# Performance work log

Measured on AMD Instinct MI355X. Metric: run time of the kernel, lower is better.

Reference implementation:

```python
import jax, jax.numpy as jnp
import numpy as np

B, S, E = 4, 2048, 512
Q, FFN = 8, 2048


def setup_inputs() -> dict:
    key = jax.random.key(0)
    k_x, k_th, k_w1, k_w2 = jax.random.split(key, 4)
    x = jax.random.normal(k_x, (B, S, E), dtype=jnp.float32)
    # trainable RY angles, one per wire
    theta = jax.random.normal(k_th, (Q,), dtype=jnp.float32)
    W1 = jax.random.normal(k_w1, (Q, FFN), dtype=jnp.float32) / np.sqrt(Q)
    b1 = jnp.zeros((FFN,), dtype=jnp.float32)
    W2 = jax.random.normal(k_w2, (FFN, E), dtype=jnp.float32) / np.sqrt(FFN)
    b2 = jnp.zeros((E,), dtype=jnp.float32)
    return {"x": x, "theta": theta, "W1": W1, "b1": b1, "W2": W2, "b2": b2}


def reference(x, theta, W1, b1, W2, b2):
    # Quantum circuit: |0> -> RX(x_i) -> RY(theta_i) -> <Z> per wire.
    # No entangling gates, so the 8-qubit state factorizes; simulate each
    # qubit's 2 complex amplitudes, batched over all tokens & wires at once.
    n_wires = theta.shape[0]
    xq = x[..., :n_wires]                     # encoder uses input_idx 0..7: [B,S,Q]
    # RX(x)|0> = cos(x/2)|0> - i sin(x/2)|1>
    a = jnp.cos(xq * 0.5).astype(jnp.complex64)
    b = (-1j) * jnp.sin(xq * 0.5).astype(jnp.complex64)
    # RY(theta) = [[c,-s],[s,c]], c=cos(theta/2), s=sin(theta/2)
    c = jnp.cos(theta * 0.5).astype(jnp.complex64)
    s = jnp.sin(theta * 0.5).astype(jnp.complex64)
    a2 = c * a - s * b
    b2_ = s * a + c * b
    # <Z> = |amp0|^2 - |amp1|^2  -> [B,S,Q]
    z = (jnp.abs(a2) ** 2 - jnp.abs(b2_) ** 2).astype(x.dtype)
    # dropout is identity at inference
    h = jax.nn.relu(jnp.einsum('bsq,qf->bsf', z, W1) + b1)
    return jnp.einsum('bsf,fe->bse', h, W2) + b2
```

## Files before the change

kernel.cpp:

```cpp
#include <hip/hip_runtime.h>
#include <hip/hip_bf16.h>

typedef __bf16 bf16_t;
typedef __bf16 bf16x4 __attribute__((ext_vector_type(4)));
typedef __bf16 bf16x8 __attribute__((ext_vector_type(8)));
typedef float f32x4 __attribute__((ext_vector_type(4)));

#define M_TOT 8192
#define N_TOT 512
#define K_TOT 2048
#define E_TOT 512
#define NSEG  16

__device__ __forceinline__ bf16x8 zero8() {
    bf16x8 v;
#pragma unroll
    for (int i = 0; i < 8; ++i) v[i] = (bf16_t)0.0f;
    return v;
}

__global__ __launch_bounds__(256)
void prep4_kernel(const float* __restrict__ x,
                  const float* __restrict__ theta,
                  const float* __restrict__ W1,
                  const float* __restrict__ b1,
                  const float* __restrict__ W2,
                  bf16_t* __restrict__ W2t,
                  bf16_t* __restrict__ zb,
                  bf16_t* __restrict__ W1p)
{
    const int b = blockIdx.x;
    if (b < 256) {
        __shared__ bf16_t T[64][66];
        const int k0 = (b >> 3) * 64;
        const int n0 = (b & 7) * 64;
        const int kl = threadIdx.x >> 4;
        const int n4 = threadIdx.x & 15;
#pragma unroll
        for (int i = 0; i < 4; ++i) {
            int k = kl + i * 16;
            float4 v = *(const float4*)(W2 + (size_t)(k0 + k) * N_TOT + n0 + n4 * 4);
            T[n4 * 4 + 0][k] = (bf16_t)v.x;
            T[n4 * 4 + 1][k] = (bf16_t)v.y;
            T[n4 * 4 + 2][k] = (bf16_t)v.z;
            T[n4 * 4 + 3][k] = (bf16_t)v.w;
        }
        __syncthreads();
        const int nl = threadIdx.x >> 4;
        const int k4 = threadIdx.x & 15;
#pragma unroll
        for (int i = 0; i < 4; ++i) {
            int n = nl + i * 16;
            bf16x4 v;
            v[0] = T[n][k4 * 4 + 0];
            v[1] = T[n][k4 * 4 + 1];
            v[2] = T[n][k4 * 4 + 2];
            v[3] = T[n][k4 * 4 + 3];
            *(bf16x4*)(W2t + (size_t)(n0 + n) * K_TOT + k0 + k4 * 4) = v;
        }
    } else if (b < 288) {
        const int m = (b - 256) * 256 + threadIdx.x;
        float4 x0 = *(const float4*)(x + (size_t)m * E_TOT);
        float4 x1 = *(const float4*)(x + (size_t)m * E_TOT + 4);
        float xs[8] = {x0.x, x0.y, x0.z, x0.w, x1.x, x1.y, x1.z, x1.w};
        bf16x8 lo;
#pragma unroll
        for (int q = 0; q < 8; ++q)
            lo[q] = (bf16_t)(__builtin_cosf(theta[q]) * __builtin_cosf(xs[q]));
        bf16x8 hi = zero8();
        hi[0] = (bf16_t)1.0f;
        *(bf16x8*)(zb + (size_t)m * 16)     = lo;
        *(bf16x8*)(zb + (size_t)m * 16 + 8) = hi;
    } else {
        const int d  = (b - 288) * 256 + threadIdx.x;
        const int c  = d >> 5;
        const int dd = d & 31;
        const int p  = dd >> 4;
        const int rr = dd & 15;
        const int f  = c * 32 + ((rr >> 2) << 3) + (p << 2) + (rr & 3);
        bf16x8 lo;
#pragma unroll
        for (int q = 0; q < 8; ++q)
            lo[q] = (bf16_t)W1[(size_t)q * K_TOT + f];
        bf16x8 hi = zero8();
        hi[0] = (bf16_t)b1[f];
        *(bf16x8*)(W1p + (size_t)d * 16)     = lo;
        *(bf16x8*)(W1p + (size_t)d * 16 + 8) = hi;
    }
}

__device__ __forceinline__ void load_B(const bf16_t* __restrict__ W2t, int n_base,
                                       int k0, int t, uint4 gv[4]) {
#pragma unroll
    for (int j = 0; j < 4; ++j) {
        int s    = t + j * 256;
        int tile = s >> 9;
        int n    = (s >> 3) & 63;
        int g    = (s & 7) ^ (n & 7);
        gv[j] = *(const uint4*)(W2t + (size_t)(n_base + n) * K_TOT
                                + k0 + tile * 64 + g * 8);
    }
}
__device__ __forceinline__ void write_B(bf16_t* Bb, int t, const uint4 gv[4]) {
#pragma unroll
    for (int j = 0; j < 4; ++j) {
        int s    = t + j * 256;
        int tile = s >> 9;
        int n    = (s >> 3) & 63;
        int seg  = s & 7;
        *(uint4*)(Bb + tile * 4096 + n * 64 + seg * 8) = gv[j];
    }
}

__device__ __forceinline__ void load_wf(const bf16_t* __restrict__ W1p, int k0,
                                        int l15, int lq, bf16x8 wf[4]) {
#pragma unroll
    for (int i = 0; i < 4; ++i) wf[i] = zero8();
    if (lq < 2) {
        const int base = (k0 >> 5) * 2;
#pragma unroll
        for (int i = 0; i < 4; ++i)
            wf[i] = *(const bf16x8*)(W1p + (size_t)((base + i) * 16 + l15) * 16 + lq * 8);
    }
}

__device__ __forceinline__ void compute_tile(const bf16_t* Bb, const bf16x8 wf[4],
                                             const bf16x8 zfrag[2],
                                             int l15, int lq,
                                             f32x4 acc[2][4]) {
    bf16x8 bfr[2][4];
#pragma unroll
    for (int c = 0; c < 2; ++c)
#pragma unroll
        for (int nt = 0; nt < 4; ++nt) {
            int r = nt * 16 + l15;
            int s = (c * 4 + lq) ^ (r & 7);
            bfr[c][nt] = *(const bf16x8*)(Bb + r * 64 + s * 8);
        }

    bf16x8 af[2][2];
#pragma unroll
    for (int mt = 0; mt < 2; ++mt)
#pragma unroll
        for (int c = 0; c < 2; ++c) {
            f32x4 h0 = (f32x4){0.f, 0.f, 0.f, 0.f};
            f32x4 h1 = (f32x4){0.f, 0.f, 0.f, 0.f};
            h0 = __builtin_amdgcn_mfma_f32_16x16x32_bf16(wf[c * 2 + 0], zfrag[mt], h0, 0, 0, 0);
            h1 = __builtin_amdgcn_mfma_f32_16x16x32_bf16(wf[c * 2 + 1], zfrag[mt], h1, 0, 0, 0);
            bf16x8 a;
#pragma unroll
            for (int r = 0; r < 4; ++r) {
                a[r]     = (bf16_t)fmaxf(h0[r], 0.f);
                a[r + 4] = (bf16_t)fmaxf(h1[r], 0.f);
            }
            af[mt][c] = a;
        }

#pragma unroll
    for (int c = 0; c < 2; ++c)
#pragma unroll
        for (int mt = 0; mt < 2; ++mt)
#pragma unroll
            for (int nt = 0; nt < 4; ++nt)
                acc[mt][nt] = __builtin_amdgcn_mfma_f32_16x16x32_bf16(
                    af[mt][c], bfr[c][nt], acc[mt][nt], 0, 0, 0);
}

__global__ __launch_bounds__(256, 2)
void ffq_gemm_kernel(const bf16_t* __restrict__ zb,
                     const bf16_t* __restrict__ W1p,
                     const bf16_t* __restrict__ W2t,
                     const float* __restrict__ b2,
                     float* __restrict__ out)
{
    __shared__ bf16_t Blds[2][2 * 64 * 64];

    const int t = threadIdx.x;
    const int w = t >> 6, l = t & 63;
    const int m_base = blockIdx.y * 128;
    const int n_base = blockIdx.x * 64;
    const int wm = w;
    const int l15 = l & 15, lq = l >> 4;

    bf16x8 zfrag[2];
#pragma unroll
    for (int mt = 0; mt < 2; ++mt) {
        zfrag[mt] = zero8();
        if (lq < 2)
            zfrag[mt] = *(const bf16x8*)(zb + (size_t)(m_base + wm * 32 + mt * 16 + l15) * 16 + lq * 8);
    }

    f32x4 acc[2][4];
#pragma unroll
    for (int mt = 0; mt < 2; ++mt)
#pragma unroll
        for (int nt = 0; nt < 4; ++nt)
            acc[mt][nt] = (f32x4){0.f, 0.f, 0.f, 0.f};

    uint4 gv[4];

    load_B(W2t, n_base, 0, t, gv);
    write_B(Blds[0], t, gv);

    for (int s = 0; s < NSEG; ++s) {
        const int cur = s & 1;
        __syncthreads();
        if (s + 1 < NSEG) load_B(W2t, n_base, (s + 1) * 128, t, gv);

#pragma unroll
        for (int tt = 0; tt < 2; ++tt) {
            bf16x8 wf[4];
            load_wf(W1p, s * 128 + tt * 64, l15, lq, wf);
            compute_tile(Blds[cur] + tt * 4096, wf, zfrag, l15, lq, acc);
        }

        if (s + 1 < NSEG) write_B(Blds[1 - cur], t, gv);
    }

#pragma unroll
    for (int nt = 0; nt < 4; ++nt) {
        int col = n_base + nt * 16 + l15;
        float bias = b2[col];
#pragma unroll
        for (int mt = 0; mt < 2; ++mt) {
#pragma unroll
            for (int r = 0; r < 4; ++r) {
                int row = m_base + wm * 32 + mt * 16 + lq * 4 + r;
                out[(size_t)row * N_TOT + col] = acc[mt][nt][r] + bias;
            }
        }
    }
}

extern "C" void kernel_launch(void* const* d_in, const int* in_sizes, int n_in,
                              void* d_out, int out_size, void* d_ws, size_t ws_size,
                              hipStream_t stream) {
    const float* x     = (const float*)d_in[0];
    const float* theta = (const float*)d_in[1];
    const float* W1    = (const float*)d_in[2];
    const float* b1    = (const float*)d_in[3];
    const float* W2    = (const float*)d_in[4];
    const float* b2    = (const float*)d_in[5];
    float* out = (float*)d_out;

    const size_t W2T_BYTES = (size_t)N_TOT * K_TOT * sizeof(bf16_t);
    const size_t ZB_BYTES  = (size_t)M_TOT * 16 * sizeof(bf16_t);

    bf16_t* W2t = (bf16_t*)d_ws;
    bf16_t* zb  = (bf16_t*)((char*)d_ws + W2T_BYTES);
    bf16_t* W1p = (bf16_t*)((char*)d_ws + W2T_BYTES + ZB_BYTES);

    prep4_kernel<<<296, 256, 0, stream>>>(x, theta, W1, b1, W2, W2t, zb, W1p);

    dim3 grid(N_TOT / 64, M_TOT / 128);
    ffq_gemm_kernel<<<grid, 256, 0, stream>>>(zb, W1p, W2t, b2, out);
}
```

Measured before the change: 107.6 us.

## Switch GEMM waves to a 2x2 layout and prefetch W1 fragments per segment

Waves are rearranged from a 4x1 split (32 rows by 64 columns each) to a 2x2 split (64 rows by 32 columns each), which halves the W2 fragment reads from LDS per wave. In exchange, each wave now recomputes the fused first-layer hidden activations for twice as many rows, raising the MFMA count per k-step. W1 fragments for the whole segment are also loaded one segment ahead into registers, double-buffered, to hide global-load latency. This increases register pressure under the existing 2-blocks-per-CU launch bound.

Result: slower. 120.7 us (+12.1%).

```diff
diff --git a/kernel.cpp b/kernel.cpp
--- a/kernel.cpp
+++ b/kernel.cpp
@@ -112,58 +112,16 @@
     }
 }
 
-__device__ __forceinline__ void load_wf(const bf16_t* __restrict__ W1p, int k0,
-                                        int l15, int lq, bf16x8 wf[4]) {
-#pragma unroll
-    for (int i = 0; i < 4; ++i) wf[i] = zero8();
+__device__ __forceinline__ void load_wf_seg(const bf16_t* __restrict__ W1p, int k0,
+                                            int l15, int lq, bf16x8 wf[8]) {
+#pragma unroll
+    for (int i = 0; i < 8; ++i) wf[i] = zero8();
     if (lq < 2) {
         const int base = (k0 >> 5) * 2;
 #pragma unroll
-        for (int i = 0; i < 4; ++i)
+        for (int i = 0; i < 8; ++i)
             wf[i] = *(const bf16x8*)(W1p + (size_t)((base + i) * 16 + l15) * 16 + lq * 8);
     }
-}
-
-__device__ __forceinline__ void compute_tile(const bf16_t* Bb, const bf16x8 wf[4],
-                                             const bf16x8 zfrag[2],
-                                             int l15, int lq,
-                                             f32x4 acc[2][4]) {
-    bf16x8 bfr[2][4];
-#pragma unroll
-    for (int c = 0; c < 2; ++c)
-#pragma unroll
-        for (int nt = 0; nt < 4; ++nt) {
-            int r = nt * 16 + l15;
-            int s = (c * 4 + lq) ^ (r & 7);
-            bfr[c][nt] = *(const bf16x8*)(Bb + r * 64 + s * 8);
-        }
-
-    bf16x8 af[2][2];
-#pragma unroll
-    for (int mt = 0; mt < 2; ++mt)
-#pragma unroll
-        for (int c = 0; c < 2; ++c) {
-            f32x4 h0 = (f32x4){0.f, 0.f, 0.f, 0.f};
-            f32x4 h1 = (f32x4){0.f, 0.f, 0.f, 0.f};
-            h0 = __builtin_amdgcn_mfma_f32_16x16x32_bf16(wf[c * 2 + 0], zfrag[mt], h0, 0, 0, 0);
-            h1 = __builtin_amdgcn_mfma_f32_16x16x32_bf16(wf[c * 2 + 1], zfrag[mt], h1, 0, 0, 0);
-            bf16x8 a;
-#pragma unroll
-            for (int r = 0; r < 4; ++r) {
-                a[r]     = (bf16_t)fmaxf(h0[r], 0.f);
-                a[r + 4] = (bf16_t)fmaxf(h1[r], 0.f);
-            }
-            af[mt][c] = a;
-        }
-
-#pragma unroll
-    for (int c = 0; c < 2; ++c)
-#pragma unroll
-        for (int mt = 0; mt < 2; ++mt)
-#pragma unroll
-            for (int nt = 0; nt < 4; ++nt)
-                acc[mt][nt] = __builtin_amdgcn_mfma_f32_16x16x32_bf16(
-                    af[mt][c], bfr[c][nt], acc[mt][nt], 0, 0, 0);
 }
 
 __global__ __launch_bounds__(256, 2)
@@ -179,53 +137,92 @@
     const int w = t >> 6, l = t & 63;
     const int m_base = blockIdx.y * 128;
     const int n_base = blockIdx.x * 64;
-    const int wm = w;
+    const int wm = w >> 1, wn = w & 1;
     const int l15 = l & 15, lq = l >> 4;
 
-    bf16x8 zfrag[2];
-#pragma unroll
-    for (int mt = 0; mt < 2; ++mt) {
+    bf16x8 zfrag[4];
+#pragma unroll
+    for (int mt = 0; mt < 4; ++mt) {
         zfrag[mt] = zero8();
         if (lq < 2)
-            zfrag[mt] = *(const bf16x8*)(zb + (size_t)(m_base + wm * 32 + mt * 16 + l15) * 16 + lq * 8);
-    }
-
-    f32x4 acc[2][4];
-#pragma unroll
-    for (int mt = 0; mt < 2; ++mt)
-#pragma unroll
-        for (int nt = 0; nt < 4; ++nt)
+            zfrag[mt] = *(const bf16x8*)(zb + (size_t)(m_base + wm * 64 + mt * 16 + l15) * 16 + lq * 8);
+    }
+
+    f32x4 acc[4][2];
+#pragma unroll
+    for (int mt = 0; mt < 4; ++mt)
+#pragma unroll
+        for (int nt = 0; nt < 2; ++nt)
             acc[mt][nt] = (f32x4){0.f, 0.f, 0.f, 0.f};
 
     uint4 gv[4];
+    bf16x8 wf_cur[8], wf_nxt[8];
 
     load_B(W2t, n_base, 0, t, gv);
+    load_wf_seg(W1p, 0, l15, lq, wf_cur);
     write_B(Blds[0], t, gv);
 
     for (int s = 0; s < NSEG; ++s) {
         const int cur = s & 1;
         __syncthreads();
-        if (s + 1 < NSEG) load_B(W2t, n_base, (s + 1) * 128, t, gv);
+        const bool more = (s + 1 < NSEG);
+        if (more) {
+            load_B(W2t, n_base, (s + 1) * 128, t, gv);
+            load_wf_seg(W1p, (s + 1) * 128, l15, lq, wf_nxt);
+        }
+
+        bf16x8 bfr[2][2][2];
+#pragma unroll
+        for (int tt = 0; tt < 2; ++tt)
+#pragma unroll
+            for (int c = 0; c < 2; ++c)
+#pragma unroll
+                for (int nt = 0; nt < 2; ++nt) {
+                    int r  = wn * 32 + nt * 16 + l15;
+                    int sg = (c * 4 + lq) ^ (r & 7);
+                    bfr[tt][c][nt] = *(const bf16x8*)(Blds[cur] + tt * 4096 + r * 64 + sg * 8);
+                }
 
 #pragma unroll
         for (int tt = 0; tt < 2; ++tt) {
-            bf16x8 wf[4];
-            load_wf(W1p, s * 128 + tt * 64, l15, lq, wf);
-            compute_tile(Blds[cur] + tt * 4096, wf, zfrag, l15, lq, acc);
-        }
-
-        if (s + 1 < NSEG) write_B(Blds[1 - cur], t, gv);
-    }
-
-#pragma unroll
-    for (int nt = 0; nt < 4; ++nt) {
-        int col = n_base + nt * 16 + l15;
+#pragma unroll
+            for (int c = 0; c < 2; ++c) {
+#pragma unroll
+                for (int mt = 0; mt < 4; ++mt) {
+                    f32x4 h0 = (f32x4){0.f, 0.f, 0.f, 0.f};
+                    f32x4 h1 = (f32x4){0.f, 0.f, 0.f, 0.f};
+                    h0 = __builtin_amdgcn_mfma_f32_16x16x32_bf16(
+                        wf_cur[tt * 4 + c * 2 + 0], zfrag[mt], h0, 0, 0, 0);
+                    h1 = __builtin_amdgcn_mfma_f32_16x16x32_bf16(
+                        wf_cur[tt * 4 + c * 2 + 1], zfrag[mt], h1, 0, 0, 0);
+                    bf16x8 af;
+#pragma unroll
+                    for (int r = 0; r < 4; ++r) {
+                        af[r]     = (bf16_t)fmaxf(h0[r], 0.f);
+                        af[r + 4] = (bf16_t)fmaxf(h1[r], 0.f);
+                    }
+#pragma unroll
+                    for (int nt = 0; nt < 2; ++nt)
+                        acc[mt][nt] = __builtin_amdgcn_mfma_f32_16x16x32_bf16(
+                            af, bfr[tt][c][nt], acc[mt][nt], 0, 0, 0);
+                }
+            }
+        }
+
+        if (more) write_B(Blds[1 - cur], t, gv);
+#pragma unroll
+        for (int i = 0; i < 8; ++i) wf_cur[i] = wf_nxt[i];
+    }
+
+#pragma unroll
+    for (int nt = 0; nt < 2; ++nt) {
+        int col = n_base + wn * 32 + nt * 16 + l15;
         float bias = b2[col];
 #pragma unroll
-        for (int mt = 0; mt < 2; ++mt) {
+        for (int mt = 0; mt < 4; ++mt) {
 #pragma unroll
             for (int r = 0; r < 4; ++r) {
-                int row = m_base + wm * 32 + mt * 16 + lq * 4 + r;
+                int row = m_base + wm * 64 + mt * 16 + lq * 4 + r;
                 out[(size_t)row * N_TOT + col] = acc[mt][nt][r] + bias;
             }
         }
```

## Split GEMM K dimension in two with atomic accumulation into zeroed output

Applied to the files above, without the earlier changes.

Splits the K=2048 reduction across two blocks per output tile (grid z=2), each covering half the segments, and merges the partials with float atomic adds into the output. The prep kernel gains extra blocks that zero the output buffer first, and only the first split adds the bias. Launch bounds are raised to request four blocks per CU, which doubles the number of blocks available to fill the GPU. The cost is an extra full-output zeroing pass plus atomic read-modify-write traffic on the output, and summation order becomes nondeterministic.

After: 119.9 us. +11.4%, slower.

```diff
diff --git a/kernel.cpp b/kernel.cpp
--- a/kernel.cpp
+++ b/kernel.cpp
@@ -10,7 +10,7 @@
 #define N_TOT 512
 #define K_TOT 2048
 #define E_TOT 512
-#define NSEG  16
+#define NSEG_HALF 8
 
 __device__ __forceinline__ bf16x8 zero8() {
     bf16x8 v;
@@ -20,16 +20,25 @@
 }
 
 __global__ __launch_bounds__(256)
-void prep4_kernel(const float* __restrict__ x,
+void prep5_kernel(const float* __restrict__ x,
                   const float* __restrict__ theta,
                   const float* __restrict__ W1,
                   const float* __restrict__ b1,
                   const float* __restrict__ W2,
                   bf16_t* __restrict__ W2t,
                   bf16_t* __restrict__ zb,
-                  bf16_t* __restrict__ W1p)
+                  bf16_t* __restrict__ W1p,
+                  float* __restrict__ out)
 {
     const int b = blockIdx.x;
+    if (b >= 296) {
+        float4* o4 = (float4*)out;
+        int idx = ((b - 296) * 256 + (int)threadIdx.x) * 2;
+        float4 z4 = {0.f, 0.f, 0.f, 0.f};
+        o4[idx] = z4;
+        o4[idx + 1] = z4;
+        return;
+    }
     if (b < 256) {
         __shared__ bf16_t T[64][66];
         const int k0 = (b >> 3) * 64;
@@ -166,7 +175,7 @@
                     af[mt][c], bfr[c][nt], acc[mt][nt], 0, 0, 0);
 }
 
-__global__ __launch_bounds__(256, 2)
+__global__ __launch_bounds__(256, 4)
 void ffq_gemm_kernel(const bf16_t* __restrict__ zb,
                      const bf16_t* __restrict__ W1p,
                      const bf16_t* __restrict__ W2t,
@@ -179,6 +188,8 @@
     const int w = t >> 6, l = t & 63;
     const int m_base = blockIdx.y * 128;
     const int n_base = blockIdx.x * 64;
+    const int kk     = blockIdx.z;
+    const int kbase  = kk * (K_TOT / 2);
     const int wm = w;
     const int l15 = l & 15, lq = l >> 4;
 
@@ -199,34 +210,35 @@
 
     uint4 gv[4];
 
-    load_B(W2t, n_base, 0, t, gv);
+    load_B(W2t, n_base, kbase, t, gv);
     write_B(Blds[0], t, gv);
 
-    for (int s = 0; s < NSEG; ++s) {
+    for (int s = 0; s < NSEG_HALF; ++s) {
         const int cur = s & 1;
         __syncthreads();
-        if (s + 1 < NSEG) load_B(W2t, n_base, (s + 1) * 128, t, gv);
+        if (s + 1 < NSEG_HALF) load_B(W2t, n_base, kbase + (s + 1) * 128, t, gv);
 
 #pragma unroll
         for (int tt = 0; tt < 2; ++tt) {
             bf16x8 wf[4];
-            load_wf(W1p, s * 128 + tt * 64, l15, lq, wf);
+            load_wf(W1p, kbase + s * 128 + tt * 64, l15, lq, wf);
             compute_tile(Blds[cur] + tt * 4096, wf, zfrag, l15, lq, acc);
         }
 
-        if (s + 1 < NSEG) write_B(Blds[1 - cur], t, gv);
+        if (s + 1 < NSEG_HALF) write_B(Blds[1 - cur], t, gv);
     }
 
 #pragma unroll
     for (int nt = 0; nt < 4; ++nt) {
         int col = n_base + nt * 16 + l15;
-        float bias = b2[col];
+        float bias = (kk == 0) ? b2[col] : 0.0f;
 #pragma unroll
         for (int mt = 0; mt < 2; ++mt) {
 #pragma unroll
             for (int r = 0; r < 4; ++r) {
                 int row = m_base + wm * 32 + mt * 16 + lq * 4 + r;
-                out[(size_t)row * N_TOT + col] = acc[mt][nt][r] + bias;
+                unsafeAtomicAdd(&out[(size_t)row * N_TOT + col],
+                                acc[mt][nt][r] + bias);
             }
         }
     }
@@ -250,8 +262,8 @@
     bf16_t* zb  = (bf16_t*)((char*)d_ws + W2T_BYTES);
     bf16_t* W1p = (bf16_t*)((char*)d_ws + W2T_BYTES + ZB_BYTES);
 
-    prep4_kernel<<<296, 256, 0, stream>>>(x, theta, W1, b1, W2, W2t, zb, W1p);
-
-    dim3 grid(N_TOT / 64, M_TOT / 128);
+    prep5_kernel<<<2344, 256, 0, stream>>>(x, theta, W1, b1, W2, W2t, zb, W1p, out);
+
+    dim3 grid(N_TOT / 64, M_TOT / 128, 2);
     ffq_gemm_kernel<<<grid, 256, 0, stream>>>(zb, W1p, W2t, b2, out);
 }
```

## Load W2 fragments directly from global into registers with intra-block split-K

Applied to the files above, without the earlier changes.

Removes the LDS double-buffered staging of W2t. Each wave now loads its MFMA B fragments straight from global memory into registers, with software prefetch of the next 64-wide K chunk. Blocks grow to 512 threads covering 256 rows: each wave handles 64 rows and half of K, and the two K halves are reduced through shared memory at the end. This cuts LDS traffic and barriers and gives more M reuse per wave. The costs are uncoalesced, row-strided global loads that depend on L2 hits, higher register pressure from double fragment buffers plus 16 accumulators, and a 64KB shared reduction buffer that may limit occupancy.

After: 118.5 us. 10.2% more time.

```diff
diff --git a/kernel.cpp b/kernel.cpp
--- a/kernel.cpp
+++ b/kernel.cpp
@@ -10,7 +10,6 @@
 #define N_TOT 512
 #define K_TOT 2048
 #define E_TOT 512
-#define NSEG  16
 
 __device__ __forceinline__ bf16x8 zero8() {
     bf16x8 v;
@@ -89,27 +88,14 @@
     }
 }
 
-__device__ __forceinline__ void load_B(const bf16_t* __restrict__ W2t, int n_base,
-                                       int k0, int t, uint4 gv[4]) {
-#pragma unroll
-    for (int j = 0; j < 4; ++j) {
-        int s    = t + j * 256;
-        int tile = s >> 9;
-        int n    = (s >> 3) & 63;
-        int g    = (s & 7) ^ (n & 7);
-        gv[j] = *(const uint4*)(W2t + (size_t)(n_base + n) * K_TOT
-                                + k0 + tile * 64 + g * 8);
-    }
-}
-__device__ __forceinline__ void write_B(bf16_t* Bb, int t, const uint4 gv[4]) {
-#pragma unroll
-    for (int j = 0; j < 4; ++j) {
-        int s    = t + j * 256;
-        int tile = s >> 9;
-        int n    = (s >> 3) & 63;
-        int seg  = s & 7;
-        *(uint4*)(Bb + tile * 4096 + n * 64 + seg * 8) = gv[j];
-    }
+__device__ __forceinline__ void load_bfr(const bf16_t* __restrict__ W2t, int n_base,
+                                         int k0, int l15, int lq, bf16x8 bfr[8]) {
+#pragma unroll
+    for (int c = 0; c < 2; ++c)
+#pragma unroll
+        for (int nt = 0; nt < 4; ++nt)
+            bfr[c * 4 + nt] = *(const bf16x8*)(W2t
+                + (size_t)(n_base + nt * 16 + l15) * K_TOT + k0 + (c * 4 + lq) * 8);
 }
 
 __device__ __forceinline__ void load_wf(const bf16_t* __restrict__ W1p, int k0,
@@ -124,23 +110,11 @@
     }
 }
 
-__device__ __forceinline__ void compute_tile(const bf16_t* Bb, const bf16x8 wf[4],
-                                             const bf16x8 zfrag[2],
-                                             int l15, int lq,
-                                             f32x4 acc[2][4]) {
-    bf16x8 bfr[2][4];
-#pragma unroll
-    for (int c = 0; c < 2; ++c)
-#pragma unroll
-        for (int nt = 0; nt < 4; ++nt) {
-            int r = nt * 16 + l15;
-            int s = (c * 4 + lq) ^ (r & 7);
-            bfr[c][nt] = *(const bf16x8*)(Bb + r * 64 + s * 8);
-        }
-
-    bf16x8 af[2][2];
-#pragma unroll
-    for (int mt = 0; mt < 2; ++mt)
+__device__ __forceinline__ void compute64(const bf16x8 bfr[8], const bf16x8 wf[4],
+                                          const bf16x8 zfrag[4], f32x4 acc[4][4]) {
+    bf16x8 af[4][2];
+#pragma unroll
+    for (int mt = 0; mt < 4; ++mt)
 #pragma unroll
         for (int c = 0; c < 2; ++c) {
             f32x4 h0 = (f32x4){0.f, 0.f, 0.f, 0.f};
@@ -155,78 +129,89 @@
             }
             af[mt][c] = a;
         }
-
 #pragma unroll
     for (int c = 0; c < 2; ++c)
 #pragma unroll
-        for (int mt = 0; mt < 2; ++mt)
+        for (int mt = 0; mt < 4; ++mt)
 #pragma unroll
             for (int nt = 0; nt < 4; ++nt)
                 acc[mt][nt] = __builtin_amdgcn_mfma_f32_16x16x32_bf16(
-                    af[mt][c], bfr[c][nt], acc[mt][nt], 0, 0, 0);
-}
-
-__global__ __launch_bounds__(256, 2)
+                    af[mt][c], bfr[c * 4 + nt], acc[mt][nt], 0, 0, 0);
+}
+
+__global__ __launch_bounds__(512, 2)
 void ffq_gemm_kernel(const bf16_t* __restrict__ zb,
                      const bf16_t* __restrict__ W1p,
                      const bf16_t* __restrict__ W2t,
                      const float* __restrict__ b2,
                      float* __restrict__ out)
 {
-    __shared__ bf16_t Blds[2][2 * 64 * 64];
+    __shared__ float Red[4][64 * 64];
 
     const int t = threadIdx.x;
     const int w = t >> 6, l = t & 63;
-    const int m_base = blockIdx.y * 128;
+    const int wm = w & 3, wk = w >> 2;
+    const int m_base = blockIdx.y * 256 + wm * 64;
     const int n_base = blockIdx.x * 64;
-    const int wm = w;
     const int l15 = l & 15, lq = l >> 4;
-
-    bf16x8 zfrag[2];
-#pragma unroll
-    for (int mt = 0; mt < 2; ++mt) {
+    const int kbase = wk * (K_TOT / 2);
+
+    bf16x8 zfrag[4];
+#pragma unroll
+    for (int mt = 0; mt < 4; ++mt) {
         zfrag[mt] = zero8();
         if (lq < 2)
-            zfrag[mt] = *(const bf16x8*)(zb + (size_t)(m_base + wm * 32 + mt * 16 + l15) * 16 + lq * 8);
-    }
-
-    f32x4 acc[2][4];
-#pragma unroll
-    for (int mt = 0; mt < 2; ++mt)
+            zfrag[mt] = *(const bf16x8*)(zb + (size_t)(m_base + mt * 16 + l15) * 16 + lq * 8);
+    }
+
+    f32x4 acc[4][4];
+#pragma unroll
+    for (int mt = 0; mt < 4; ++mt)
 #pragma unroll
         for (int nt = 0; nt < 4; ++nt)
             acc[mt][nt] = (f32x4){0.f, 0.f, 0.f, 0.f};
 
-    uint4 gv[4];
-
-    load_B(W2t, n_base, 0, t, gv);
-    write_B(Blds[0], t, gv);
-
-    for (int s = 0; s < NSEG; ++s) {
-        const int cur = s & 1;
-        __syncthreads();
-        if (s + 1 < NSEG) load_B(W2t, n_base, (s + 1) * 128, t, gv);
-
-#pragma unroll
-        for (int tt = 0; tt < 2; ++tt) {
-            bf16x8 wf[4];
-            load_wf(W1p, s * 128 + tt * 64, l15, lq, wf);
-            compute_tile(Blds[cur] + tt * 4096, wf, zfrag, l15, lq, acc);
-        }
-
-        if (s + 1 < NSEG) write_B(Blds[1 - cur], t, gv);
-    }
-
-#pragma unroll
-    for (int nt = 0; nt < 4; ++nt) {
-        int col = n_base + nt * 16 + l15;
-        float bias = b2[col];
-#pragma unroll
-        for (int mt = 0; mt < 2; ++mt) {
-#pragma unroll
-            for (int r = 0; r < 4; ++r) {
-                int row = m_base + wm * 32 + mt * 16 + lq * 4 + r;
-                out[(size_t)row * N_TOT + col] = acc[mt][nt][r] + bias;
+    bf16x8 bfrA[8], bfrB[8], wfA[4], wfB[4];
+
+    load_bfr(W2t, n_base, kbase, l15, lq, bfrA);
+    load_wf(W1p, kbase, l15, lq, wfA);
+
+    for (int kt = 0; kt < 16; kt += 2) {
+        const int k0 = kbase + kt * 64;
+        load_bfr(W2t, n_base, k0 + 64, l15, lq, bfrB);
+        load_wf(W1p, k0 + 64, l15, lq, wfB);
+        compute64(bfrA, wfA, zfrag, acc);
+
+        if (kt + 2 < 16) {
+            load_bfr(W2t, n_base, k0 + 128, l15, lq, bfrA);
+            load_wf(W1p, k0 + 128, l15, lq, wfA);
+        }
+        compute64(bfrB, wfB, zfrag, acc);
+    }
+
+    if (wk == 1) {
+#pragma unroll
+        for (int mt = 0; mt < 4; ++mt)
+#pragma unroll
+            for (int nt = 0; nt < 4; ++nt)
+#pragma unroll
+                for (int r = 0; r < 4; ++r)
+                    Red[wm][(mt * 16 + lq * 4 + r) * 64 + nt * 16 + l15] = acc[mt][nt][r];
+    }
+    __syncthreads();
+    if (wk == 0) {
+#pragma unroll
+        for (int nt = 0; nt < 4; ++nt) {
+            int col = n_base + nt * 16 + l15;
+            float bias = b2[col];
+#pragma unroll
+            for (int mt = 0; mt < 4; ++mt) {
+#pragma unroll
+                for (int r = 0; r < 4; ++r) {
+                    int row = m_base + mt * 16 + lq * 4 + r;
+                    out[(size_t)row * N_TOT + col] = acc[mt][nt][r] + bias
+                        + Red[wm][(mt * 16 + lq * 4 + r) * 64 + nt * 16 + l15];
+                }
             }
         }
     }
@@ -252,6 +237,6 @@
 
     prep4_kernel<<<296, 256, 0, stream>>>(x, theta, W1, b1, W2, W2t, zb, W1p);
 
-    dim3 grid(N_TOT / 64, M_TOT / 128);
-    ffq_gemm_kernel<<<grid, 256, 0, stream>>>(zb, W1p, W2t, b2, out);
-}
+    dim3 grid(N_TOT / 64, M_TOT / 256);
+    ffq_gemm_kernel<<<grid, 512, 0, stream>>>(zb, W1p, W2t, b2, out);
+}
```
